# Kernel optimization log

Measured on AMD Instinct MI355X. Metric: run time of the kernel, lower is better.

Reference implementation:

```python
import jax, jax.numpy as jnp
import numpy as np


def setup_inputs() -> dict:
    key = jax.random.key(0)
    ks = jax.random.split(key, 8)
    b, l, d_model = 2, 2048, 1024
    d_inner, d_state, dt_rank, d_conv = 2048, 16, 64, 4
    g = lambda k, shape, s: jax.random.normal(k, shape, jnp.float32) * s
    A = jnp.broadcast_to(jnp.arange(1, d_state + 1, dtype=jnp.float32), (d_inner, d_state))
    return {
        "x": g(ks[0], (b, l, d_model), 1.0),
        "W_in": g(ks[1], (d_model, 2 * d_inner), 0.02),
        "W_conv": g(ks[2], (d_inner, 1, d_conv), 0.1),
        "b_conv": g(ks[3], (d_inner,), 0.1),
        "W_x": g(ks[4], (d_inner, dt_rank + 2 * d_state), 0.02),
        "W_dt": g(ks[5], (dt_rank, d_inner), 0.02),
        "b_dt": g(ks[6], (d_inner,), 0.1),
        "A_log": jnp.log(A),
        "D": jnp.ones((d_inner,), jnp.float32),
        "W_out": g(ks[7], (d_inner, d_model), 0.02),
    }


def _selective_scan(x, delta, A, B, C, D):
    # x, delta: (b, l, d); A: (d, n); B, C: (b, l, n); D: (d,)
    b, l, d = x.shape
    n = A.shape[1]

    def step(h, inp):
        dt, Bt, Ct, xt = inp  # (b,d), (b,n), (b,n), (b,d)
        dA = jnp.exp(dt[:, :, None] * A)                     # (b,d,n)
        h = dA * h + (dt * xt)[:, :, None] * Bt[:, None, :]  # (b,d,n)
        y = jnp.einsum('bdn,bn->bd', h, Ct)
        return h, y

    h0 = jnp.zeros((b, d, n), x.dtype)
    xs = (jnp.swapaxes(delta, 0, 1), jnp.swapaxes(B, 0, 1),
          jnp.swapaxes(C, 0, 1), jnp.swapaxes(x, 0, 1))
    _, ys = jax.lax.scan(step, h0, xs)   # ys: (l, b, d)
    return jnp.swapaxes(ys, 0, 1) + D * x


def _mamba(x, W_in, W_conv, b_conv, W_x, W_dt, b_dt, A_log, D, W_out):
    b, l, _ = x.shape
    d_inner = W_conv.shape[0]
    d_conv = W_conv.shape[2]
    dt_rank = W_dt.shape[0]
    n = A_log.shape[1]

    xr = x @ W_in                                   # (b,l,2*d_inner)
    xin, res = xr[..., :d_inner], xr[..., d_inner:]

    # depthwise causal conv1d (left pad d_conv-1 == torch pad both + trim to l)
    xc = jnp.swapaxes(xin, 1, 2)                    # (b,d_inner,l)
    xc = jax.lax.conv_general_dilated(
        xc, W_conv, window_strides=(1,), padding=[(d_conv - 1, 0)],
        feature_group_count=d_inner,
        dimension_numbers=('NCH', 'OIH', 'NCH')) + b_conv[None, :, None]
    xs = jax.nn.silu(jnp.swapaxes(xc, 1, 2))        # (b,l,d_inner)

    x_dbl = xs @ W_x                                # (b,l,dt_rank+2n)
    delta = jax.nn.softplus(x_dbl[..., :dt_rank] @ W_dt + b_dt)
    Bm = x_dbl[..., dt_rank:dt_rank + n]
    Cm = x_dbl[..., dt_rank + n:]
    A = -jnp.exp(A_log)

    y = _selective_scan(xs, delta, A, Bm, Cm, D)
    y = y * jax.nn.silu(res)
    return y @ W_out


def reference(x, W_in, W_conv, b_conv, W_x, W_dt, b_dt, A_log, D, W_out):
    return _mamba(x, W_in, W_conv, b_conv, W_x, W_dt, b_dt, A_log, D, W_out)
```

## Files before the change

kernel.cpp:

```cpp
#include <hip/hip_runtime.h>


typedef unsigned short ushort_t;
using short8 = __attribute__((ext_vector_type(8))) short;
using f32x4  = __attribute__((ext_vector_type(4))) float;
using gptr_t = const __attribute__((address_space(1))) unsigned short*;
using sptr_t = __attribute__((address_space(3))) unsigned short*;

#define NC 64
#define CL 32

__device__ inline ushort_t f2bf(float v) {
    unsigned u = __float_as_uint(v);
    unsigned r = (u + 0x7fff + ((u >> 16) & 1)) >> 16;
    return (ushort_t)r;
}
__device__ inline float bf2f(ushort_t h) { return __uint_as_float(((unsigned)h) << 16); }
__device__ inline void split2(float v, ushort_t& h, ushort_t& l) {
    h = f2bf(v);
    l = f2bf(v - bf2f(h));
}

__global__ __launch_bounds__(256) void convert_all(
    const float* __restrict__ x, ushort_t* __restrict__ xh, ushort_t* __restrict__ xl,
    const float* __restrict__ W_in, ushort_t* __restrict__ winh, ushort_t* __restrict__ winl,
    const float* __restrict__ W_out, ushort_t* __restrict__ wouth, ushort_t* __restrict__ woutl,
    const float* __restrict__ W_x, ushort_t* __restrict__ wxh, ushort_t* __restrict__ wxl,
    const float* __restrict__ W_dt, ushort_t* __restrict__ wdth, ushort_t* __restrict__ wdtl) {
    __shared__ float tile[32][33];
    const int id = blockIdx.x;
    if (id < 4096) {
        int i = id * 256 + threadIdx.x;
        float4 v = ((const float4*)x)[i];
        ushort4 hh, ll;
        split2(v.x, hh.x, ll.x); split2(v.y, hh.y, ll.y);
        split2(v.z, hh.z, ll.z); split2(v.w, hh.w, ll.w);
        ((ushort4*)xh)[i] = hh;
        ((ushort4*)xl)[i] = ll;
        return;
    }
    const float* W; ushort_t *Th, *Tl; int K, N, bx, by;
    if (id < 8192)       { W = W_in;  Th = winh;  Tl = winl;  K = 1024; N = 4096;
                           bx = (id - 4096) & 127; by = (id - 4096) >> 7; }
    else if (id < 10240) { W = W_out; Th = wouth; Tl = woutl; K = 2048; N = 1024;
                           bx = (id - 8192) & 31;  by = (id - 8192) >> 5; }
    else if (id < 10496) { W = W_x;   Th = wxh;   Tl = wxl;   K = 2048; N = 96;
                           bx = (id - 10240) & 3;  by = (id - 10240) >> 2; }
    else                 { W = W_dt;  Th = wdth;  Tl = wdtl;  K = 64;   N = 2048;
                           bx = (id - 10496) & 63; by = (id - 10496) >> 6; }
    int n0 = bx * 32, k0 = by * 32;
    int tx = threadIdx.x & 31, ty = threadIdx.x >> 5;
    #pragma unroll
    for (int j = 0; j < 4; ++j) {
        int k = ty + j * 8;
        tile[k][tx] = (n0 + tx < N) ? W[(size_t)(k0 + k) * N + n0 + tx] : 0.f;
    }
    __syncthreads();
    #pragma unroll
    for (int j = 0; j < 4; ++j) {
        int nrow = ty + j * 8;
        float v = tile[tx][nrow];
        ushort_t h, l;
        split2(v, h, l);
        size_t o = (size_t)(n0 + nrow) * K + k0 + tx;
        Th[o] = h; Tl[o] = l;
    }
}

__global__ __launch_bounds__(256) void gemm_mfma3(
    const ushort_t* __restrict__ Ah, const ushort_t* __restrict__ Al,
    const ushort_t* __restrict__ Bh, const ushort_t* __restrict__ Bl,
    float* __restrict__ C, int M, int N, int K,
    const float* __restrict__ bias, int epi) {
    __shared__ ushort_t sAh[4096], sAl[4096], sBh[4096], sBl[4096];
    const int tid  = threadIdx.x;
    const int wid  = tid >> 6;
    const int lane = tid & 63;
    const int bm = blockIdx.y * 128;
    const int bn = blockIdx.x * 128;
    const int wr = wid >> 1, wc = wid & 1;

    f32x4 acc[4][4];
    #pragma unroll
    for (int i = 0; i < 4; ++i)
        #pragma unroll
        for (int j = 0; j < 4; ++j) acc[i][j] = (f32x4){0.f, 0.f, 0.f, 0.f};

    for (int k0 = 0; k0 < K; k0 += 32) {
        #pragma unroll
        for (int issue = 0; issue < 2; ++issue) {
            const int off = wid * 2048 + issue * 1024 + lane * 16;
            const int row = off >> 6;
            const int ce  = (off & 63) >> 1;
            const size_t ga = (size_t)(bm + row) * K + k0 + ce;
            const size_t gb = (size_t)(bn + row) * K + k0 + ce;
            const int lo = (wid * 2048 + issue * 1024) >> 1;
            __builtin_amdgcn_global_load_lds((gptr_t)(Ah + ga), (sptr_t)&sAh[lo], 16, 0, 0);
            __builtin_amdgcn_global_load_lds((gptr_t)(Al + ga), (sptr_t)&sAl[lo], 16, 0, 0);
            __builtin_amdgcn_global_load_lds((gptr_t)(Bh + gb), (sptr_t)&sBh[lo], 16, 0, 0);
            __builtin_amdgcn_global_load_lds((gptr_t)(Bl + gb), (sptr_t)&sBl[lo], 16, 0, 0);
        }
        __syncthreads();

        const int fr = lane & 15;
        const int kb = (lane >> 4) * 8;
        short8 ah[4], al[4], bh[4], bl[4];
        #pragma unroll
        for (int i = 0; i < 4; ++i) {
            const int ra = (wr * 64 + i * 16 + fr) * 32 + kb;
            ah[i] = *(const short8*)&sAh[ra];
            al[i] = *(const short8*)&sAl[ra];
            const int rb = (wc * 64 + i * 16 + fr) * 32 + kb;
            bh[i] = *(const short8*)&sBh[rb];
            bl[i] = *(const short8*)&sBl[rb];
        }
        #pragma unroll
        for (int i = 0; i < 4; ++i)
            #pragma unroll
            for (int j = 0; j < 4; ++j) {
                acc[i][j] = __builtin_amdgcn_mfma_f32_16x16x32_bf16(ah[i], bh[j], acc[i][j], 0, 0, 0);
                acc[i][j] = __builtin_amdgcn_mfma_f32_16x16x32_bf16(ah[i], bl[j], acc[i][j], 0, 0, 0);
                acc[i][j] = __builtin_amdgcn_mfma_f32_16x16x32_bf16(al[i], bh[j], acc[i][j], 0, 0, 0);
            }
        __syncthreads();
    }

    #pragma unroll
    for (int i = 0; i < 4; ++i) {
        int row = bm + wr * 64 + i * 16 + (lane >> 4) * 4;
        #pragma unroll
        for (int j = 0; j < 4; ++j) {
            int col = bn + wc * 64 + j * 16 + (lane & 15);
            float* cp = C + (size_t)row * N + col;
            #pragma unroll
            for (int r = 0; r < 4; ++r) {
                float v = acc[i][j][r];
                if (epi == 1) {
                    v += bias[col];
                    v = (v > 20.f) ? v : log1pf(__expf(v));
                }
                cp[(size_t)r * N] = v;
            }
        }
    }
}

__global__ __launch_bounds__(256) void gemm_mfma3_n64(
    const ushort_t* __restrict__ Ah, const ushort_t* __restrict__ Al,
    const ushort_t* __restrict__ Bh, const ushort_t* __restrict__ Bl,
    float* __restrict__ C, int M, int N, int K) {
    __shared__ ushort_t sAh[4096], sAl[4096], sBh[2048], sBl[2048];
    const int tid  = threadIdx.x;
    const int wid  = tid >> 6;
    const int lane = tid & 63;
    const int bm = blockIdx.y * 128;
    const int bn = blockIdx.x * 64;
    const int wr = wid >> 1, wc = wid & 1;

    f32x4 acc[4][2];
    #pragma unroll
    for (int i = 0; i < 4; ++i)
        #pragma unroll
        for (int j = 0; j < 2; ++j) acc[i][j] = (f32x4){0.f, 0.f, 0.f, 0.f};

    for (int k0 = 0; k0 < K; k0 += 32) {
        #pragma unroll
        for (int issue = 0; issue < 2; ++issue) {
            const int off = issue * 4096 + tid * 16;
            const int row = off >> 6;
            const int ce  = (off & 63) >> 1;
            const size_t ga = (size_t)(bm + row) * K + k0 + ce;
            const int lo = (issue * 4096 + wid * 1024) >> 1;
            __builtin_amdgcn_global_load_lds((gptr_t)(Ah + ga), (sptr_t)&sAh[lo], 16, 0, 0);
            __builtin_amdgcn_global_load_lds((gptr_t)(Al + ga), (sptr_t)&sAl[lo], 16, 0, 0);
        }
        {
            const int off = tid * 16;
            const int row = off >> 6;
            const int ce  = (off & 63) >> 1;
            const size_t gb = (size_t)(bn + row) * K + k0 + ce;
            const int lo = (wid * 1024) >> 1;
            __builtin_amdgcn_global_load_lds((gptr_t)(Bh + gb), (sptr_t)&sBh[lo], 16, 0, 0);
            __builtin_amdgcn_global_load_lds((gptr_t)(Bl + gb), (sptr_t)&sBl[lo], 16, 0, 0);
        }
        __syncthreads();

        const int fr = lane & 15;
        const int kb = (lane >> 4) * 8;
        short8 ah[4], al[4], bh[2], bl[2];
        #pragma unroll
        for (int i = 0; i < 4; ++i) {
            const int ra = (wr * 64 + i * 16 + fr) * 32 + kb;
            ah[i] = *(const short8*)&sAh[ra];
            al[i] = *(const short8*)&sAl[ra];
        }
        #pragma unroll
        for (int j = 0; j < 2; ++j) {
            const int rb = (wc * 32 + j * 16 + fr) * 32 + kb;
            bh[j] = *(const short8*)&sBh[rb];
            bl[j] = *(const short8*)&sBl[rb];
        }
        #pragma unroll
        for (int i = 0; i < 4; ++i)
            #pragma unroll
            for (int j = 0; j < 2; ++j) {
                acc[i][j] = __builtin_amdgcn_mfma_f32_16x16x32_bf16(ah[i], bh[j], acc[i][j], 0, 0, 0);
                acc[i][j] = __builtin_amdgcn_mfma_f32_16x16x32_bf16(ah[i], bl[j], acc[i][j], 0, 0, 0);
                acc[i][j] = __builtin_amdgcn_mfma_f32_16x16x32_bf16(al[i], bh[j], acc[i][j], 0, 0, 0);
            }
        __syncthreads();
    }

    #pragma unroll
    for (int i = 0; i < 4; ++i) {
        int row = bm + wr * 64 + i * 16 + (lane >> 4) * 4;
        #pragma unroll
        for (int j = 0; j < 2; ++j) {
            int col = bn + wc * 32 + j * 16 + (lane & 15);
            float* cp = C + (size_t)row * N + col;
            #pragma unroll
            for (int r = 0; r < 4; ++r) cp[(size_t)r * N] = acc[i][j][r];
        }
    }
}

__global__ __launch_bounds__(256) void gemm_mfma3_sk(
    const ushort_t* __restrict__ Ah, const ushort_t* __restrict__ Al,
    const ushort_t* __restrict__ Bh, const ushort_t* __restrict__ Bl,
    float* __restrict__ partial, int K) {
    __shared__ ushort_t sAh[4096], sAl[4096], sBh[4096], sBl[4096];
    const int tid  = threadIdx.x;
    const int wid  = tid >> 6;
    const int lane = tid & 63;
    const int kslice = blockIdx.x;
    const int bm = blockIdx.y * 128;
    const int wr = wid >> 1, wc = wid & 1;
    const int kbeg = kslice * 128;

    f32x4 acc[4][4];
    #pragma unroll
    for (int i = 0; i < 4; ++i)
        #pragma unroll
        for (int j = 0; j < 4; ++j) acc[i][j] = (f32x4){0.f, 0.f, 0.f, 0.f};

    for (int k0 = kbeg; k0 < kbeg + 128; k0 += 32) {
        #pragma unroll
        for (int issue = 0; issue < 2; ++issue) {
            const int off = wid * 2048 + issue * 1024 + lane * 16;
            const int row = off >> 6;
            const int ce  = (off & 63) >> 1;
            const size_t ga = (size_t)(bm + row) * K + k0 + ce;
            const size_t gb = (size_t)row * K + k0 + ce;
            const int lo = (wid * 2048 + issue * 1024) >> 1;
            __builtin_amdgcn_global_load_lds((gptr_t)(Ah + ga), (sptr_t)&sAh[lo], 16, 0, 0);
            __builtin_amdgcn_global_load_lds((gptr_t)(Al + ga), (sptr_t)&sAl[lo], 16, 0, 0);
            __builtin_amdgcn_global_load_lds((gptr_t)(Bh + gb), (sptr_t)&sBh[lo], 16, 0, 0);
            __builtin_amdgcn_global_load_lds((gptr_t)(Bl + gb), (sptr_t)&sBl[lo], 16, 0, 0);
        }
        __syncthreads();

        const int fr = lane & 15;
        const int kb = (lane >> 4) * 8;
        short8 ah[4], al[4], bh[4], bl[4];
        #pragma unroll
        for (int i = 0; i < 4; ++i) {
            const int ra = (wr * 64 + i * 16 + fr) * 32 + kb;
            ah[i] = *(const short8*)&sAh[ra];
            al[i] = *(const short8*)&sAl[ra];
            const int rb = (wc * 64 + i * 16 + fr) * 32 + kb;
            bh[i] = *(const short8*)&sBh[rb];
            bl[i] = *(const short8*)&sBl[rb];
        }
        #pragma unroll
        for (int i = 0; i < 4; ++i)
            #pragma unroll
            for (int j = 0; j < 4; ++j) {
                acc[i][j] = __builtin_amdgcn_mfma_f32_16x16x32_bf16(ah[i], bh[j], acc[i][j], 0, 0, 0);
                acc[i][j] = __builtin_amdgcn_mfma_f32_16x16x32_bf16(ah[i], bl[j], acc[i][j], 0, 0, 0);
                acc[i][j] = __builtin_amdgcn_mfma_f32_16x16x32_bf16(al[i], bh[j], acc[i][j], 0, 0, 0);
            }
        __syncthreads();
    }

    float* Cp = partial + (size_t)kslice * 4096 * 96;
    #pragma unroll
    for (int i = 0; i < 4; ++i) {
        int row = bm + wr * 64 + i * 16 + (lane >> 4) * 4;
        #pragma unroll
        for (int j = 0; j < 4; ++j) {
            int col = wc * 64 + j * 16 + (lane & 15);
            if (col < 96) {
                float* cp = Cp + (size_t)row * 96 + col;
                #pragma unroll
                for (int r = 0; r < 4; ++r) cp[(size_t)r * 96] = acc[i][j][r];
            }
        }
    }
}

__global__ void reduce16split(const float4* __restrict__ p, float4* __restrict__ xdbl4,
                              ushort_t* __restrict__ dh, ushort_t* __restrict__ dl) {
    int i = blockIdx.x * 256 + threadIdx.x;
    float4 s = p[i];
    #pragma unroll
    for (int k = 1; k < 16; ++k) {
        float4 v = p[i + k * 98304];
        s.x += v.x; s.y += v.y; s.z += v.z; s.w += v.w;
    }
    int row = i / 24;
    int c4  = i - row * 24;
    xdbl4[row * 32 + c4] = s;
    if (c4 < 16) {
        ushort4 hh, ll;
        split2(s.x, hh.x, ll.x); split2(s.y, hh.y, ll.y);
        split2(s.z, hh.z, ll.z); split2(s.w, hh.w, ll.w);
        ((ushort4*)dh)[row * 16 + c4] = hh;
        ((ushort4*)dl)[row * 16 + c4] = ll;
    }
}

__global__ void conv_silu_k(const float* __restrict__ xr, const float* __restrict__ Wc,
                            const float* __restrict__ bc,
                            ushort_t* __restrict__ xsh, ushort_t* __restrict__ xsl,
                            int total) {
    for (int idx = blockIdx.x * blockDim.x + threadIdx.x; idx < total;
         idx += gridDim.x * blockDim.x) {
        int d = idx & 2047;
        int l = (idx >> 11) & 2047;
        int b = idx >> 22;
        float acc = bc[d];
        const float* wp = Wc + d * 4;
        #pragma unroll
        for (int k = 0; k < 4; ++k) {
            int ll = l - 3 + k;
            if (ll >= 0)
                acc = fmaf(xr[((size_t)(b * 2048 + ll) << 12) + d], wp[k], acc);
        }
        float v = acc / (1.f + __expf(-acc));
        ushort_t h, lo;
        split2(v, h, lo);
        xsh[idx] = h;
        xsl[idx] = lo;
    }
}


__global__ __launch_bounds__(256) void scan_p1(
    const float* __restrict__ delta,
    const ushort_t* __restrict__ xsh, const ushort_t* __restrict__ xsl,
    const float* __restrict__ xdbl, const float* __restrict__ A_log,
    float* __restrict__ S, float* __restrict__ sumdt) {
    const int u = blockIdx.x * 256 + threadIdx.x;
    const int chunk = u >> 12;
    const int c = u & 4095;
    const int b = c >> 11, d = c & 2047;

    float a[16];
    #pragma unroll
    for (int i = 0; i < 4; ++i) {
        float4 v = ((const float4*)(A_log + d * 16))[i];
        a[4 * i + 0] = -__expf(v.x); a[4 * i + 1] = -__expf(v.y);
        a[4 * i + 2] = -__expf(v.z); a[4 * i + 3] = -__expf(v.w);
    }
    float h[16];
    #pragma unroll
    for (int n = 0; n < 16; ++n) h[n] = 0.f;
    float sdt = 0.f;

    const size_t row0 = (size_t)b * 2048 + (size_t)chunk * CL;
    const float4* xd4 = (const float4*)xdbl;
    #pragma unroll 2
    for (int t = 0; t < CL; ++t) {
        const size_t row = row0 + t;
        float dt = delta[row * 2048 + d];
        float xv = bf2f(xsh[row * 2048 + d]) + bf2f(xsl[row * 2048 + d]);
        float4 Bv[4];
        #pragma unroll
        for (int i = 0; i < 4; ++i) Bv[i] = xd4[row * 32 + 16 + i];
        const float* Bf = (const float*)Bv;
        sdt += dt;
        float du = dt * xv;
        #pragma unroll
        for (int n = 0; n < 16; ++n) {
            float dA = __expf(dt * a[n]);
            h[n] = fmaf(dA, h[n], du * Bf[n]);
        }
    }
    float4* S4 = (float4*)(S + ((size_t)chunk * 4096 + c) * 16);
    #pragma unroll
    for (int i = 0; i < 4; ++i)
        S4[i] = make_float4(h[4 * i + 0], h[4 * i + 1], h[4 * i + 2], h[4 * i + 3]);
    sumdt[chunk * 4096 + c] = sdt;
}

__global__ __launch_bounds__(256) void scan_p2(
    float* __restrict__ S, const float* __restrict__ sumdt,
    const float* __restrict__ A_log) {
    const int idx = blockIdx.x * blockDim.x + threadIdx.x;
    const int n = idx & 15;
    const int c = (idx >> 4) & 4095;
    const int d = c & 2047;
    const float a = -__expf(A_log[d * 16 + n]);
    float h = 0.f;
    for (int k = 0; k < NC; ++k) {
        const size_t o = ((size_t)k * 4096 + c) * 16 + n;
        float carry = S[o];
        S[o] = h;
        float P = __expf(a * sumdt[k * 4096 + c]);
        h = fmaf(P, h, carry);
    }
}

__global__ __launch_bounds__(256) void scan_p3(
    const float* __restrict__ delta,
    const ushort_t* __restrict__ xsh, const ushort_t* __restrict__ xsl,
    const float* __restrict__ xdbl, const float* __restrict__ xr,
    const float* __restrict__ A_log, const float* __restrict__ Dp,
    const float* __restrict__ H0,
    ushort_t* __restrict__ yh, ushort_t* __restrict__ yl) {
    const int u = blockIdx.x * 256 + threadIdx.x;
    const int chunk = u >> 12;
    const int c = u & 4095;
    const int b = c >> 11, d = c & 2047;

    float a[16];
    #pragma unroll
    for (int i = 0; i < 4; ++i) {
        float4 v = ((const float4*)(A_log + d * 16))[i];
        a[4 * i + 0] = -__expf(v.x); a[4 * i + 1] = -__expf(v.y);
        a[4 * i + 2] = -__expf(v.z); a[4 * i + 3] = -__expf(v.w);
    }
    float h[16];
    const float4* H4 = (const float4*)(H0 + ((size_t)chunk * 4096 + c) * 16);
    #pragma unroll
    for (int i = 0; i < 4; ++i) {
        float4 v = H4[i];
        h[4 * i + 0] = v.x; h[4 * i + 1] = v.y; h[4 * i + 2] = v.z; h[4 * i + 3] = v.w;
    }
    const float Dd = Dp[d];

    const size_t row0 = (size_t)b * 2048 + (size_t)chunk * CL;
    const float4* xd4 = (const float4*)xdbl;
    #pragma unroll 2
    for (int t = 0; t < CL; ++t) {
        const size_t row = row0 + t;
        float dt = delta[row * 2048 + d];
        float xv = bf2f(xsh[row * 2048 + d]) + bf2f(xsl[row * 2048 + d]);
        float4 BC[8];
        #pragma unroll
        for (int i = 0; i < 8; ++i) BC[i] = xd4[row * 32 + 16 + i];
        const float* Bf = (const float*)BC;
        const float* Cf = Bf + 16;
        float du = dt * xv;
        float acc = 0.f;
        #pragma unroll
        for (int n = 0; n < 16; ++n) {
            float dA = __expf(dt * a[n]);
            h[n] = fmaf(dA, h[n], du * Bf[n]);
            acc = fmaf(h[n], Cf[n], acc);
        }
        float rv = xr[(row << 12) + 2048 + d];
        float yv = fmaf(Dd, xv, acc) * (rv / (1.f + __expf(-rv)));
        ushort_t hb, lb;
        split2(yv, hb, lb);
        yh[row * 2048 + d] = hb;
        yl[row * 2048 + d] = lb;
    }
}

extern "C" void kernel_launch(void* const* d_in, const int* in_sizes, int n_in,
                              void* d_out, int out_size, void* d_ws, size_t ws_size,
                              hipStream_t stream) {
    const float* x      = (const float*)d_in[0];
    const float* W_in   = (const float*)d_in[1];
    const float* W_conv = (const float*)d_in[2];
    const float* b_conv = (const float*)d_in[3];
    const float* W_x    = (const float*)d_in[4];
    const float* W_dt   = (const float*)d_in[5];
    const float* b_dt   = (const float*)d_in[6];
    const float* A_log  = (const float*)d_in[7];
    const float* Dp     = (const float*)d_in[8];
    const float* W_out  = (const float*)d_in[9];
    float* out = (float*)d_out;

    float* ws    = (float*)d_ws;
    float* xr    = ws;
    float* xdbl  = xr + 16777216;
    float* delta = xdbl + 524288;
    float* S     = delta + 8388608;
    float* sumdt = S + 4194304;
    ushort_t* base = (ushort_t*)(sumdt + 262144);
    ushort_t* xh = base, *xl = base + 4194304;
    ushort_t* winh = base + 8388608, *winl = base + 12582912;
    float*    partial = (float*)base;
    ushort_t* yh = base, *yl = base + 8388608;
    ushort_t* wouth = base + 16777216, *woutl = base + 18874368;
    ushort_t* wxh   = base + 20971520, *wxl   = base + 21233664;
    ushort_t* wdth  = base + 21495808, *wdtl  = base + 21626880;
    ushort_t* dAh   = base + 21757952, *dAl   = base + 22020096;
    ushort_t* xsh   = base + 22282240, *xsl   = base + 30670848;

    dim3 blk(256);

    convert_all<<<dim3(10624), blk, 0, stream>>>(x, xh, xl, W_in, winh, winl,
                                                 W_out, wouth, woutl,
                                                 W_x, wxh, wxl, W_dt, wdth, wdtl);

    gemm_mfma3<<<dim3(32, 32), blk, 0, stream>>>(xh, xl, winh, winl, xr,
                                                 4096, 4096, 1024, nullptr, 0);
    conv_silu_k<<<dim3(4096), blk, 0, stream>>>(xr, W_conv, b_conv, xsh, xsl, 8388608);
    gemm_mfma3_sk<<<dim3(16, 32), blk, 0, stream>>>(xsh, xsl, wxh, wxl, partial, 2048);
    reduce16split<<<dim3(384), blk, 0, stream>>>((const float4*)partial, (float4*)xdbl,
                                                 dAh, dAl);
    gemm_mfma3<<<dim3(16, 32), blk, 0, stream>>>(dAh, dAl, wdth, wdtl, delta,
                                                 4096, 2048, 64, b_dt, 1);
    scan_p1<<<dim3(1024), blk, 0, stream>>>(delta, xsh, xsl, xdbl, A_log, S, sumdt);
    scan_p2<<<dim3(256), blk, 0, stream>>>(S, sumdt, A_log);
    scan_p3<<<dim3(1024), blk, 0, stream>>>(delta, xsh, xsl, xdbl, xr, A_log, Dp, S, yh, yl);
    gemm_mfma3_n64<<<dim3(16, 32), blk, 0, stream>>>(yh, yl, wouth, woutl, out,
                                                     4096, 1024, 2048);
}
```

Baseline: 525.5 us.

## Use 256x256-tile 512-thread split-bf16 GEMM for input projection

Replaces the 128x128 in-projection GEMM with a new 256x256 tile kernel using 8 waves, direct global-to-LDS loads, XOR-swizzled LDS layout, double buffering and split-phase MFMA with priority hints. The aim is more operand reuse per LDS load and overlap of loads with compute for the largest GEMM. The trade-offs are 128KB of LDS per block, high register pressure from 32 accumulators, and only 256 blocks covering the CUs.

```diff
diff --git a/kernel.cpp b/kernel.cpp
--- a/kernel.cpp
+++ b/kernel.cpp
@@ -67,6 +67,131 @@
     }
 }
 
+__global__ __launch_bounds__(512, 2) void gemm_mfma3_256(
+    const ushort_t* __restrict__ Ah, const ushort_t* __restrict__ Al,
+    const ushort_t* __restrict__ Bh, const ushort_t* __restrict__ Bl,
+    float* __restrict__ C, int M, int N, int K) {
+    __shared__ ushort_t lds[65536];
+    const int tid  = threadIdx.x;
+    const int w    = tid >> 6;
+    const int lane = tid & 63;
+    const int wr = w >> 2;
+    const int wc = w & 3;
+    const int fr = lane & 15;
+    const int kq = (lane >> 4) * 8;
+    const int bm = blockIdx.y * 256;
+    const int bn = blockIdx.x * 256;
+    const int NT = K >> 5;
+
+    const int sg   = tid ^ ((tid >> 3) & 7);
+    const int srow = sg >> 2;
+    const int skof = (sg & 3) * 8;
+
+    f32x4 acc[8][4];
+    #pragma unroll
+    for (int i = 0; i < 8; ++i)
+        #pragma unroll
+        for (int j = 0; j < 4; ++j) acc[i][j] = (f32x4){0.f, 0.f, 0.f, 0.f};
+
+    #define STAGE(t, db)                                                          \
+    {                                                                             \
+        const int k0_ = (t) * 32;                                                 \
+        _Pragma("unroll")                                                         \
+        for (int h_ = 0; h_ < 2; ++h_) {                                          \
+            const size_t ga_ = (size_t)(bm + h_ * 128 + srow) * K + k0_ + skof;   \
+            const size_t gb_ = (size_t)(bn + h_ * 128 + srow) * K + k0_ + skof;   \
+            const int dst_ = (db) * 8192 + h_ * 4096 + w * 512;                   \
+            __builtin_amdgcn_global_load_lds((gptr_t)(Ah + ga_), (sptr_t)&lds[0     + dst_], 16, 0, 0); \
+            __builtin_amdgcn_global_load_lds((gptr_t)(Al + ga_), (sptr_t)&lds[16384 + dst_], 16, 0, 0); \
+            __builtin_amdgcn_global_load_lds((gptr_t)(Bh + gb_), (sptr_t)&lds[32768 + dst_], 16, 0, 0); \
+            __builtin_amdgcn_global_load_lds((gptr_t)(Bl + gb_), (sptr_t)&lds[49152 + dst_], 16, 0, 0); \
+        }                                                                         \
+    }
+
+    #define LDF(arrOff, db, row) \
+        (*(const short8*)&lds[(arrOff) + (db) * 8192 + \
+            ((((row) << 2) | (kq >> 3)) ^ (((row) >> 1) & 7)) * 8])
+
+    STAGE(0, 0);
+    STAGE(1, 1);
+    asm volatile("s_waitcnt vmcnt(8)" ::: "memory");
+    __builtin_amdgcn_s_barrier();
+
+    for (int t = 0; t < NT; ++t) {
+        const int db = t & 1;
+        short8 bhF[4], blF[4], ahF[4], alF[4];
+        #pragma unroll
+        for (int j = 0; j < 4; ++j) {
+            const int row = 128 + wc * 32 + j * 16 + fr - 128;
+            (void)row;
+        }
+        #pragma unroll
+        for (int j = 0; j < 4; ++j) {
+            const int rowb = wc * 64 + j * 16 + fr;
+            bhF[j] = LDF(32768, db, rowb);
+            blF[j] = LDF(49152, db, rowb);
+        }
+        #pragma unroll
+        for (int i = 0; i < 4; ++i) {
+            const int rowa = wr * 128 + i * 16 + fr;
+            ahF[i] = LDF(0, db, rowa);
+            alF[i] = LDF(16384, db, rowa);
+        }
+        __builtin_amdgcn_s_setprio(1);
+        #pragma unroll
+        for (int i = 0; i < 4; ++i)
+            #pragma unroll
+            for (int j = 0; j < 4; ++j) {
+                acc[i][j] = __builtin_amdgcn_mfma_f32_16x16x32_bf16(ahF[i], bhF[j], acc[i][j], 0, 0, 0);
+                acc[i][j] = __builtin_amdgcn_mfma_f32_16x16x32_bf16(ahF[i], blF[j], acc[i][j], 0, 0, 0);
+                acc[i][j] = __builtin_amdgcn_mfma_f32_16x16x32_bf16(alF[i], bhF[j], acc[i][j], 0, 0, 0);
+            }
+        __builtin_amdgcn_s_setprio(0);
+        short8 ah2[4], al2[4];
+        #pragma unroll
+        for (int i = 0; i < 4; ++i) {
+            const int rowa = wr * 128 + (i + 4) * 16 + fr;
+            ah2[i] = LDF(0, db, rowa);
+            al2[i] = LDF(16384, db, rowa);
+        }
+        asm volatile("s_waitcnt lgkmcnt(0)" ::: "memory");
+        __builtin_amdgcn_sched_barrier(0);
+        __builtin_amdgcn_s_barrier();
+        if (t + 2 < NT) STAGE(t + 2, db);
+        __builtin_amdgcn_s_setprio(1);
+        #pragma unroll
+        for (int i = 0; i < 4; ++i)
+            #pragma unroll
+            for (int j = 0; j < 4; ++j) {
+                acc[i + 4][j] = __builtin_amdgcn_mfma_f32_16x16x32_bf16(ah2[i], bhF[j], acc[i + 4][j], 0, 0, 0);
+                acc[i + 4][j] = __builtin_amdgcn_mfma_f32_16x16x32_bf16(ah2[i], blF[j], acc[i + 4][j], 0, 0, 0);
+                acc[i + 4][j] = __builtin_amdgcn_mfma_f32_16x16x32_bf16(al2[i], bhF[j], acc[i + 4][j], 0, 0, 0);
+            }
+        __builtin_amdgcn_s_setprio(0);
+        if (t + 2 < NT) {
+            asm volatile("s_waitcnt vmcnt(8)" ::: "memory");
+        } else {
+            asm volatile("s_waitcnt vmcnt(0)" ::: "memory");
+        }
+        __builtin_amdgcn_sched_barrier(0);
+        __builtin_amdgcn_s_barrier();
+    }
+    #undef STAGE
+    #undef LDF
+
+    #pragma unroll
+    for (int i = 0; i < 8; ++i) {
+        const int row = bm + wr * 128 + i * 16 + (lane >> 4) * 4;
+        #pragma unroll
+        for (int j = 0; j < 4; ++j) {
+            const int col = bn + wc * 64 + j * 16 + fr;
+            float* cp = C + (size_t)row * N + col;
+            #pragma unroll
+            for (int r = 0; r < 4; ++r) cp[(size_t)r * N] = acc[i][j][r];
+        }
+    }
+}
+
 __global__ __launch_bounds__(256) void gemm_mfma3(
     const ushort_t* __restrict__ Ah, const ushort_t* __restrict__ Al,
     const ushort_t* __restrict__ Bh, const ushort_t* __restrict__ Bl,
@@ -343,7 +468,6 @@
         xsl[idx] = lo;
     }
 }
-
 
 __global__ __launch_bounds__(256) void scan_p1(
     const float* __restrict__ delta,
@@ -506,8 +630,8 @@
                                                  W_out, wouth, woutl,
                                                  W_x, wxh, wxl, W_dt, wdth, wdtl);
 
-    gemm_mfma3<<<dim3(32, 32), blk, 0, stream>>>(xh, xl, winh, winl, xr,
-                                                 4096, 4096, 1024, nullptr, 0);
+    gemm_mfma3_256<<<dim3(16, 16), dim3(512), 0, stream>>>(xh, xl, winh, winl, xr,
+                                                           4096, 4096, 1024);
     conv_silu_k<<<dim3(4096), blk, 0, stream>>>(xr, W_conv, b_conv, xsh, xsl, 8388608);
     gemm_mfma3_sk<<<dim3(16, 32), blk, 0, stream>>>(xsh, xsl, wxh, wxl, partial, 2048);
     reduce16split<<<dim3(384), blk, 0, stream>>>((const float4*)partial, (float4*)xdbl,
```

New measurement: 509.3 us. 1.03x faster.
